# Performance work log

Hardware: AMD Instinct MI355X
Metric: run time of the kernel (lower is better)

Reference implementation:

```python
import jax, jax.numpy as jnp
import numpy as np
from functools import partial

EPS = 1e-5
TOP_K = 1
NUM_EXPERTS = 3
LOSS_COEF = 0.01


def conv2d(x, w, stride, pad):
    return jax.lax.conv_general_dilated(
        x, w, (stride, stride), [(pad, pad), (pad, pad)],
        dimension_numbers=("NCHW", "OIHW", "NCHW"))


def setup_inputs() -> dict:
    key = jax.random.key(0)
    ks = jax.random.split(key, 8)
    b, c, t, h, w = 8, 3, 5, 512, 512
    E = NUM_EXPERTS
    s = 0.05  # small init scale
    return {
        "x": jax.random.normal(ks[0], (b, c, t, h, w), jnp.float32),
        "g_conv_w": jax.random.normal(ks[1], (64, 15, 7, 7), jnp.float32) * s,
        "g_bn_gamma": jnp.ones((64,), jnp.float32),
        "g_bn_beta": jnp.zeros((64,), jnp.float32),
        "g_bn_mean": jnp.zeros((64,), jnp.float32),
        "g_bn_var": jnp.ones((64,), jnp.float32),
        "g_fc_w": jax.random.normal(ks[2], (E, 64), jnp.float32) * s,
        "g_fc_b": jnp.zeros((E,), jnp.float32),
        "e_conv1_w": jax.random.normal(ks[3], (E, 64, 15, 7, 7), jnp.float32) * s,
        "e_conv2_w": jax.random.normal(ks[4], (E, 128, 64, 3, 3), jnp.float32) * s,
        "e_head_w1": jax.random.normal(ks[5], (E, 128, 128, 3, 3), jnp.float32) * s,
        "e_head_b1": jnp.zeros((E, 128), jnp.float32),
        "e_head_w2": jax.random.normal(ks[6], (E, 5, 128, 1, 1), jnp.float32) * s,
        "e_head_b2": jnp.zeros((E, 5), jnp.float32),
    }


def gating(xr, g_conv_w, g_bn_gamma, g_bn_beta, g_bn_mean, g_bn_var, g_fc_w, g_fc_b):
    # backbone: conv 7x7 s2 -> BN (eval) -> ReLU -> maxpool 3x3 s2 -> GAP -> fc
    f = conv2d(xr, g_conv_w, 2, 3)
    scale = g_bn_gamma / jnp.sqrt(g_bn_var + EPS)
    f = f * scale[None, :, None, None] + (g_bn_beta - g_bn_mean * scale)[None, :, None, None]
    f = jax.nn.relu(f)
    f = jax.lax.reduce_window(f, -jnp.inf, jax.lax.max, (1, 1, 3, 3), (1, 1, 2, 2),
                              [(0, 0), (0, 0), (1, 1), (1, 1)])
    pooled = f.mean(axis=(2, 3))                       # (b, 64)
    logits = pooled @ g_fc_w.T + g_fc_b                # (b, E)
    b = logits.shape[0]
    _, top_idx = jax.lax.top_k(logits, TOP_K)          # (b, k)
    rows = jnp.arange(b)[:, None]
    # eval-mode gating: uniform 1/k over selected experts
    sparse_gates = jnp.zeros_like(logits).at[rows, top_idx].set(1.0 / TOP_K)
    expert_mask = jnp.zeros_like(logits).at[rows, top_idx].set(1.0)
    density = expert_mask.mean(axis=0)
    density_proxy = jax.nn.softmax(logits, axis=1).mean(axis=0)
    aux_loss = (density * density_proxy).sum() * NUM_EXPERTS
    return sparse_gates, aux_loss


def expert_forward(xr, w1, w2, hw1, hb1, hw2, hb2):
    y = jax.nn.relu(conv2d(xr, w1, 2, 3))              # (b, 64, H/2, W/2)
    y = jax.nn.relu(conv2d(y, w2, 2, 1))               # (b, 128, H/4, W/4)
    y = jax.nn.relu(conv2d(y, hw1, 1, 1) + hb1[None, :, None, None])
    y = conv2d(y, hw2, 1, 0) + hb2[None, :, None, None]  # (b, 5, H/4, W/4)
    return y


def reference(x, g_conv_w, g_bn_gamma, g_bn_beta, g_bn_mean, g_bn_var, g_fc_w, g_fc_b,
              e_conv1_w, e_conv2_w, e_head_w1, e_head_b1, e_head_w2, e_head_b2):
    b, c, t, h, w = x.shape
    xr = x.reshape(b, c * t, h, w)
    sparse_gates, aux_loss = gating(xr, g_conv_w, g_bn_gamma, g_bn_beta,
                                    g_bn_mean, g_bn_var, g_fc_w, g_fc_b)
    # run all experts (gates are 0 for unselected -> identical math to sparse dispatch)
    outs = jax.vmap(lambda w1, w2, hw1, hb1, hw2, hb2:
                    expert_forward(xr, w1, w2, hw1, hb1, hw2, hb2))(
        e_conv1_w, e_conv2_w, e_head_w1, e_head_b1, e_head_w2, e_head_b2)  # (E,b,5,h4,w4)
    combined = jnp.einsum("ebchw,be->bchw", outs, sparse_gates)
    hm, wh, reg = combined[:, 0:1], combined[:, 1:3], combined[:, 3:5]
    return hm, wh, reg, LOSS_COEF * aux_loss
```

## Files before the change

kernel.cpp:

```cpp
#include <hip/hip_runtime.h>
#include <cstdint>
#include <cmath>


typedef _Float16 f16x8 __attribute__((ext_vector_type(8)));
typedef _Float16 f16x4 __attribute__((ext_vector_type(4)));
typedef float f32x4 __attribute__((ext_vector_type(4)));

__device__ __forceinline__ void g2l16(const void* g, void* l) {
  __builtin_amdgcn_global_load_lds((__attribute__((address_space(1))) void*)g,
                                   (__attribute__((address_space(3))) void*)l,
                                   16, 0, 0);
}

__device__ __forceinline__ int xcd_swz(int bid, int nwg) {
  return (bid & 7) * (nwg >> 3) + (bid >> 3);
}

__global__ __launch_bounds__(256) void prep_x_k(
    const float* __restrict__ x, _Float16* __restrict__ xp)
{
  const int t = blockIdx.x * 256 + threadIdx.x;
  const int pix = t & 262143;
  const int b   = t >> 18;
  const float* src = x + (size_t)b * 15 * 262144 + pix;
  f16x8 lo, hi;
#pragma unroll
  for (int c = 0; c < 8; ++c)  lo[c] = (_Float16)src[(size_t)c * 262144];
#pragma unroll
  for (int c = 8; c < 15; ++c) hi[c - 8] = (_Float16)src[(size_t)c * 262144];
  hi[7] = (_Float16)0.f;
  *(f16x8*)&xp[(size_t)t * 16]     = lo;
  *(f16x8*)&xp[(size_t)t * 16 + 8] = hi;
}

__global__ __launch_bounds__(256) void prep_w7_k(
    const float* __restrict__ gw, const float* __restrict__ ew,
    _Float16* __restrict__ wp)
{
  const int i = blockIdx.x * 256 + threadIdx.x;
  const int kk   = i & 31;
  const int cout = (i >> 5) & 63;
  const int pair = (i >> 11) & 3;
  const int v    = i >> 13;
  const int ky = v % 7, set = v / 7;
  const int t = kk >> 4, cin = kk & 15;
  const int kx = 2 * pair + t;
  float val = 0.f;
  if (cin < 15 && kx < 7) {
    if (set == 0) val = gw[((cout * 15 + cin) * 7 + ky) * 7 + kx];
    else          val = ew[((((set - 1) * 64 + cout) * 15 + cin) * 7 + ky) * 7 + kx];
  }
  wp[i] = (_Float16)val;
}

template<int CINC>
__global__ __launch_bounds__(256) void prep_w3_k(
    const float* __restrict__ w, _Float16* __restrict__ wp)
{
  constexpr int CH = CINC / 32;
  const int i = blockIdx.x * 256 + threadIdx.x;
  const int kk   = i & 31;
  const int cout = (i >> 5) & 127;
  int rest = i >> 12;
  const int ch  = rest % CH;  rest /= CH;
  const int tap = rest % 9;
  const int e   = rest / 9;
  const int cin = ch * 32 + kk;
  wp[i] = (_Float16)w[((size_t)(e * 128 + cout) * CINC + cin) * 9 + tap];
}

template<int MODE>
__global__ __launch_bounds__(256, 3) void conv7m_k(
    const _Float16* __restrict__ xp, const _Float16* __restrict__ wp,
    const float* __restrict__ bn_g, const float* __restrict__ bn_b,
    const float* __restrict__ bn_m, const float* __restrict__ bn_v,
    const int* __restrict__ sel, _Float16* __restrict__ out)
{
  constexpr int ROWF = 518 * 16;
  __shared__ __align__(16) _Float16 smem[18432];
  const int sb = xcd_swz(blockIdx.x, 2048);
  const int oy = sb & 255, b = sb >> 8;
  const int wv = threadIdx.x >> 6, lane = threadIdx.x & 63;
  const int ln15 = lane & 15, quad = lane >> 4;
  const int npx0 = wv * 64;

  int set = 0;
  if constexpr (MODE == 1) set = 1 + sel[b];
  const _Float16* wset = wp + (size_t)set * (7 * 4 * 64 * 32);
  const _Float16* xb   = xp + (size_t)b * (512 * 512 * 16);

  const _Float16* xrow[7];
  bool rowok[7];
#pragma unroll
  for (int ky = 0; ky < 7; ++ky) {
    const int iy = 2 * oy - 3 + ky;
    rowok[ky] = (unsigned)iy < 512u;
    const int iyc = iy < 0 ? 0 : (iy > 511 ? 511 : iy);
    xrow[ky] = xb + (size_t)iyc * (512 * 16);
  }

  if (threadIdx.x < 32) {
    const int bi = threadIdx.x >> 4, k = threadIdx.x & 15;
    if (k < 12) {
      const int g = (k < 6) ? k : (1030 + k - 6);
      f16x8 z = {};
      *(f16x8*)&smem[bi * ROWF + g * 8] = z;
    }
  }

  f32x4 acc[4][4];
#pragma unroll
  for (int f = 0; f < 4; ++f)
#pragma unroll
    for (int g = 0; g < 4; ++g) acc[f][g] = (f32x4){0.f, 0.f, 0.f, 0.f};

  auto load_af = [&](int t, f16x8* af) {
    const int ky = t >> 2, pair = t & 3;
    const _Float16* wt = wset + (size_t)((ky * 4 + pair) * 64) * 32;
#pragma unroll
    for (int f = 0; f < 4; ++f)
      af[f] = *(const f16x8*)&wt[(f * 16 + ln15) * 32 + quad * 8];
  };
  auto stage = [&](int ky, int bi) {
    _Float16* bufb = &smem[bi * ROWF];
    const _Float16* xr = xrow[ky];
#pragma unroll
    for (int s = 0; s < 4; ++s) {
      const int seg = wv * 4 + s;
      const int gl = 6 + seg * 64 + lane;
      const int gs = gl ^ ((gl >> 3) & 7);
      g2l16(xr + (size_t)((gs >> 1) - 3) * 16 + (gs & 1) * 8,
            bufb + (6 + seg * 64) * 8);
    }
  };

  int gb[4];
#pragma unroll
  for (int g = 0; g < 4; ++g)
    gb[g] = 4 * (npx0 + g * 16 + ln15) + quad;

  f16x8 afb[3][4];
  load_af(0, afb[0]);
  load_af(1, afb[1]);
  stage(0, 0);
  __syncthreads();

#pragma unroll
  for (int t = 0; t < 28; ++t) {
    const int ky = t >> 2, pair = t & 3;
    const int cur = ky & 1;
    if (t + 2 < 28) load_af(t + 2, afb[(t + 2) % 3]);
    if (pair == 0 && ky + 1 < 7) stage(ky + 1, cur ^ 1);
    if (rowok[ky]) {
      const _Float16* bufb = &smem[cur * ROWF];
#pragma unroll
      for (int g = 0; g < 4; ++g) {
        const int gq = gb[g] + 4 * pair;
        const int gs = gq ^ ((gq >> 3) & 7);
        const f16x8 bf = *(const f16x8*)&bufb[gs * 8];
#pragma unroll
        for (int f = 0; f < 4; ++f)
          acc[f][g] = __builtin_amdgcn_mfma_f32_16x16x32_f16(afb[t % 3][f], bf, acc[f][g], 0, 0, 0);
      }
    }
    if (pair == 3) __syncthreads();
  }

  _Float16* sw = &smem[wv * 4608];
#pragma unroll
  for (int f = 0; f < 4; ++f) {
    float scl[4], add[4];
#pragma unroll
    for (int r = 0; r < 4; ++r) {
      const int cout = f * 16 + quad * 4 + r;
      if constexpr (MODE == 0) {
        const float sc = bn_g[cout] * rsqrtf(bn_v[cout] + 1e-5f);
        scl[r] = sc; add[r] = bn_b[cout] - bn_m[cout] * sc;
      } else { scl[r] = 1.f; add[r] = 0.f; }
    }
#pragma unroll
    for (int g = 0; g < 4; ++g) {
      f16x4 h;
#pragma unroll
      for (int r = 0; r < 4; ++r)
        h[r] = (_Float16)fmaxf(acc[f][g][r] * scl[r] + add[r], 0.f);
      *(f16x4*)&sw[(g * 16 + ln15) * 72 + f * 16 + quad * 4] = h;
    }
  }
  __syncthreads();
  const size_t rowbase = ((size_t)(b * 256 + oy) * 256 + npx0) * 64;
#pragma unroll
  for (int i = 0; i < 8; ++i) {
    const int pxl = (lane >> 3) + i * 8;
    const int c8  = (lane & 7) * 8;
    const f16x8 v = *(const f16x8*)&sw[pxl * 72 + c8];
    *(f16x8*)&out[rowbase + (size_t)pxl * 64 + c8] = v;
  }
}

template<int CINC, int S, int INSZ, int OUTSZ, int MODE>
__global__ __launch_bounds__(256, 3) void conv3m_k(
    const _Float16* __restrict__ xp, const _Float16* __restrict__ wp,
    const float* __restrict__ p_bias, const int* __restrict__ sel,
    _Float16* __restrict__ out)
{
  constexpr int CH  = CINC / 32;
  constexpr int NCH = 3 * CH;
  constexpr int NT  = NCH * 3;
  constexpr int NPX = (S == 1) ? (OUTSZ + 2) : (2 * OUTSZ + 1);
  constexpr int ROWF = NPX * 32;
  constexpr int NGR  = NPX * 4;
  constexpr int SPW  = INSZ / 64;
  __shared__ __align__(16) _Float16 smem[18432];
  const int sb = xcd_swz(blockIdx.x, OUTSZ * 8);
  const int oy = sb % OUTSZ, b = sb / OUTSZ;
  const int wv = threadIdx.x >> 6, lane = threadIdx.x & 63;
  const int ln15 = lane & 15, quad = lane >> 4;
  const int mwb = (wv >> 1) * 64, nwb = (wv & 1) * 64;

  const int e = sel[b];
  const _Float16* we = wp + (size_t)e * (9 * CH * 128 * 32);
  const _Float16* xb = xp + (size_t)b * ((size_t)INSZ * INSZ * CINC);

  const _Float16* xrow[3];
  bool rowok[3];
#pragma unroll
  for (int ky = 0; ky < 3; ++ky) {
    const int iy = S * oy + ky - 1;
    rowok[ky] = (unsigned)iy < (unsigned)INSZ;
    const int iyc = iy < 0 ? 0 : (iy >= INSZ ? INSZ - 1 : iy);
    xrow[ky] = xb + (size_t)iyc * INSZ * CINC;
  }

  {
    constexpr int HGPB = (S == 1) ? 8 : 4;
    if (threadIdx.x < 2 * HGPB) {
      const int bi = threadIdx.x / HGPB, k = threadIdx.x % HGPB;
      const int g = (k < 4) ? k : (NGR - 8 + k);
      f16x8 z = {};
      *(f16x8*)&smem[bi * ROWF + g * 8] = z;
    }
  }

  f32x4 acc[4][4];
#pragma unroll
  for (int f = 0; f < 4; ++f)
#pragma unroll
    for (int g = 0; g < 4; ++g) acc[f][g] = (f32x4){0.f, 0.f, 0.f, 0.f};

  auto load_af = [&](int t, f16x8* af) {
    const int c = t / 3, kx = t % 3;
    const int ky = c / CH, ch = c % CH;
    const _Float16* wt = we + (size_t)(((ky * 3 + kx) * CH + ch) * 128) * 32;
#pragma unroll
    for (int f = 0; f < 4; ++f)
      af[f] = *(const f16x8*)&wt[(mwb + f * 16 + ln15) * 32 + quad * 8];
  };
  auto stage = [&](int c, int bi) {
    const int ky = c / CH, ch = c % CH;
    _Float16* bufb = &smem[bi * ROWF];
    const _Float16* xr = xrow[ky];
#pragma unroll
    for (int s = 0; s < SPW; ++s) {
      const int seg = wv * SPW + s;
      const int gl = 4 + seg * 64 + lane;
      const int gs = gl ^ ((gl >> 3) & 7);
      g2l16(xr + (size_t)((gs >> 2) - 1) * CINC + ch * 32 + (gs & 3) * 8,
            bufb + (4 + seg * 64) * 8);
    }
  };

  int gb[4];
#pragma unroll
  for (int g = 0; g < 4; ++g) {
    const int ox = nwb + g * 16 + ln15;
    gb[g] = 4 * S * ox + quad;
  }

  f16x8 afb[3][4];
  load_af(0, afb[0]);
  load_af(1, afb[1]);
  stage(0, 0);
  __syncthreads();

#pragma unroll
  for (int t = 0; t < NT; ++t) {
    const int c = t / 3, kx = t % 3;
    const int ky = c / CH;
    const int cur = c & 1;
    if (t + 2 < NT) load_af(t + 2, afb[(t + 2) % 3]);
    if (kx == 0 && c + 1 < NCH) stage(c + 1, cur ^ 1);
    if (rowok[ky]) {
      const _Float16* bufb = &smem[cur * ROWF];
#pragma unroll
      for (int g = 0; g < 4; ++g) {
        const int gq = gb[g] + 4 * kx;
        const int gs = gq ^ ((gq >> 3) & 7);
        const f16x8 bf = *(const f16x8*)&bufb[gs * 8];
#pragma unroll
        for (int f = 0; f < 4; ++f)
          acc[f][g] = __builtin_amdgcn_mfma_f32_16x16x32_f16(afb[t % 3][f], bf, acc[f][g], 0, 0, 0);
      }
    }
    if (kx == 2) __syncthreads();
  }

  _Float16* sw = &smem[wv * 4608];
#pragma unroll
  for (int f = 0; f < 4; ++f) {
#pragma unroll
    for (int g = 0; g < 4; ++g) {
      f16x4 h;
#pragma unroll
      for (int r = 0; r < 4; ++r) {
        const int cout = mwb + f * 16 + quad * 4 + r;
        float v = acc[f][g][r];
        if constexpr (MODE == 2) v += p_bias[e * 128 + cout];
        h[r] = (_Float16)fmaxf(v, 0.f);
      }
      *(f16x4*)&sw[(g * 16 + ln15) * 72 + f * 16 + quad * 4] = h;
    }
  }
  __syncthreads();
  const size_t rowbase = ((size_t)(b * OUTSZ + oy) * OUTSZ + nwb) * 128 + mwb;
#pragma unroll
  for (int i = 0; i < 8; ++i) {
    const int pxl = (lane >> 3) + i * 8;
    const int c8  = (lane & 7) * 8;
    const f16x8 v = *(const f16x8*)&sw[pxl * 72 + c8];
    *(f16x8*)&out[rowbase + (size_t)pxl * 128 + c8] = v;
  }
}

__global__ void zero_k(float* __restrict__ pooled) {
  if (threadIdx.x < 512) pooled[threadIdx.x] = 0.f;
}

__global__ __launch_bounds__(256) void pool_k(
    const _Float16* __restrict__ f, float* __restrict__ pooled)
{
  const int sb = xcd_swz(blockIdx.x, 1024);
  const int b  = sb >> 7;
  const int py = sb & 127;
  const int wv = threadIdx.x >> 6, lane = threadIdx.x & 63;
  const int c8  = (lane & 7) * 8;
  const int pxq = lane >> 3;
  const _Float16* fb = f + (size_t)b * 256 * 256 * 64;

  const int y0 = 2 * py - 1;
  float s[8];
#pragma unroll
  for (int j = 0; j < 8; ++j) s[j] = 0.f;

#pragma unroll
  for (int step = 0; step < 4; ++step) {
    const int px = wv * 32 + step * 8 + pxq;
    const int x0 = 2 * px - 1;
    f16x8 m;
#pragma unroll
    for (int j = 0; j < 8; ++j) m[j] = (_Float16)(-60000.f);
#pragma unroll
    for (int dy = 0; dy < 3; ++dy) {
      const int y = y0 + dy;
      if ((unsigned)y < 256u) {
        const _Float16* row = fb + (size_t)y * 256 * 64 + c8;
        if (x0 >= 0)
          m = __builtin_elementwise_max(m, *(const f16x8*)&row[(size_t)x0 * 64]);
        m = __builtin_elementwise_max(m, *(const f16x8*)&row[(size_t)(x0 + 1) * 64]);
        m = __builtin_elementwise_max(m, *(const f16x8*)&row[(size_t)(x0 + 2) * 64]);
      }
    }
#pragma unroll
    for (int j = 0; j < 8; ++j) s[j] += (float)m[j];
  }

  __shared__ float red[256][8];
#pragma unroll
  for (int j = 0; j < 8; ++j) red[threadIdx.x][j] = s[j];
  __syncthreads();
  if (threadIdx.x < 64) {
    const int c = threadIdx.x, cg = c >> 3, cj = c & 7;
    float t = 0.f;
#pragma unroll
    for (int k = 0; k < 32; ++k)
      t += red[(k >> 3) * 64 + (k & 7) * 8 + cg][cj];
    atomicAdd(&pooled[b * 64 + c], t);
  }
}

__global__ __launch_bounds__(64) void gate_k(
    const float* __restrict__ pooled, const float* __restrict__ fcw,
    const float* __restrict__ fcb, int* __restrict__ sel, float* __restrict__ out_aux)
{
  __shared__ float probs[8][3];
  __shared__ int sidx[8];
  const int b = threadIdx.x;
  if (b < 8) {
    float l[3];
#pragma unroll
    for (int e = 0; e < 3; ++e) {
      float s = fcb[e];
      for (int c = 0; c < 64; ++c)
        s = fmaf(pooled[b * 64 + c] * (1.f / 16384.f), fcw[e * 64 + c], s);
      l[e] = s;
    }
    int best = 0;
    if (l[1] > l[best]) best = 1;
    if (l[2] > l[best]) best = 2;
    sel[b] = best;
    sidx[b] = best;
    const float m = fmaxf(l[0], fmaxf(l[1], l[2]));
    const float e0 = expf(l[0] - m), e1 = expf(l[1] - m), e2 = expf(l[2] - m);
    const float inv = 1.f / (e0 + e1 + e2);
    probs[b][0] = e0 * inv; probs[b][1] = e1 * inv; probs[b][2] = e2 * inv;
  }
  __syncthreads();
  if (threadIdx.x == 0) {
    float cnt[3] = {0.f, 0.f, 0.f}, pr[3] = {0.f, 0.f, 0.f};
    for (int bb = 0; bb < 8; ++bb) {
      cnt[sidx[bb]] += 1.f;
#pragma unroll
      for (int e = 0; e < 3; ++e) pr[e] += probs[bb][e];
    }
    float aux = 0.f;
#pragma unroll
    for (int e = 0; e < 3; ++e) aux += (cnt[e] * 0.125f) * (pr[e] * 0.125f);
    *out_aux = 0.01f * (3.f * aux);
  }
}

__global__ __launch_bounds__(256) void head2m_k(
    const _Float16* __restrict__ in, const float* __restrict__ w,
    const float* __restrict__ b2, const int* __restrict__ sel,
    float* __restrict__ out)
{
  const int b = blockIdx.x >> 6;
  const int p = ((blockIdx.x & 63) << 8) + threadIdx.x;
  const int e = sel[b];
  const float* wp = w + (size_t)e * 5 * 128;
  const _Float16* ip = in + ((size_t)(b << 14) + p) * 128;
  float a0 = 0.f, a1 = 0.f, a2 = 0.f, a3 = 0.f, a4 = 0.f;
#pragma unroll
  for (int cc = 0; cc < 16; ++cc) {
    const f16x8 v8 = *(const f16x8*)&ip[cc * 8];
#pragma unroll
    for (int j = 0; j < 8; ++j) {
      const float v = (float)v8[j];
      const int c = cc * 8 + j;
      a0 = fmaf(v, wp[c], a0);
      a1 = fmaf(v, wp[128 + c], a1);
      a2 = fmaf(v, wp[256 + c], a2);
      a3 = fmaf(v, wp[384 + c], a3);
      a4 = fmaf(v, wp[512 + c], a4);
    }
  }
  a0 += b2[e * 5 + 0]; a1 += b2[e * 5 + 1]; a2 += b2[e * 5 + 2];
  a3 += b2[e * 5 + 3]; a4 += b2[e * 5 + 4];
  out[(b << 14) + p] = a0;
  out[131072 + ((b * 2 + 0) << 14) + p] = a1;
  out[131072 + ((b * 2 + 1) << 14) + p] = a2;
  out[393216 + ((b * 2 + 0) << 14) + p] = a3;
  out[393216 + ((b * 2 + 1) << 14) + p] = a4;
}

extern "C" void kernel_launch(void* const* d_in, const int* in_sizes, int n_in,
                              void* d_out, int out_size, void* d_ws, size_t ws_size,
                              hipStream_t stream) {
  const float* x          = (const float*)d_in[0];
  const float* g_conv_w   = (const float*)d_in[1];
  const float* g_bn_gamma = (const float*)d_in[2];
  const float* g_bn_beta  = (const float*)d_in[3];
  const float* g_bn_mean  = (const float*)d_in[4];
  const float* g_bn_var   = (const float*)d_in[5];
  const float* g_fc_w     = (const float*)d_in[6];
  const float* g_fc_b     = (const float*)d_in[7];
  const float* e_conv1_w  = (const float*)d_in[8];
  const float* e_conv2_w  = (const float*)d_in[9];
  const float* e_head_w1  = (const float*)d_in[10];
  const float* e_head_b1  = (const float*)d_in[11];
  const float* e_head_w2  = (const float*)d_in[12];
  const float* e_head_b2  = (const float*)d_in[13];
  float* out = (float*)d_out;

  _Float16* xp      = (_Float16*)d_ws;
  _Float16* featbuf = xp + 33554432;
  _Float16* y2      = featbuf + 33554432;
  _Float16* w7p     = y2 + 16777216;
  _Float16* w2p     = w7p + 229376;
  _Float16* w3p     = w2p + 221184;
  _Float16* y3      = xp;
  float*    pooled  = (float*)(w3p + 442368);
  int*      sel     = (int*)(pooled + 512);

  prep_x_k<<<8192, 256, 0, stream>>>(x, xp);
  prep_w7_k<<<896, 256, 0, stream>>>(g_conv_w, e_conv1_w, w7p);
  prep_w3_k<64><<<864, 256, 0, stream>>>(e_conv2_w, w2p);
  prep_w3_k<128><<<1728, 256, 0, stream>>>(e_head_w1, w3p);
  zero_k<<<1, 512, 0, stream>>>(pooled);

  conv7m_k<0><<<2048, 256, 0, stream>>>(xp, w7p, g_bn_gamma, g_bn_beta,
                                        g_bn_mean, g_bn_var, nullptr, featbuf);
  pool_k<<<1024, 256, 0, stream>>>(featbuf, pooled);
  gate_k<<<1, 64, 0, stream>>>(pooled, g_fc_w, g_fc_b, sel, out + 655360);

  conv7m_k<1><<<2048, 256, 0, stream>>>(xp, w7p, nullptr, nullptr, nullptr, nullptr,
                                        sel, featbuf);
  conv3m_k<64, 2, 256, 128, 1><<<1024, 256, 0, stream>>>(featbuf, w2p, nullptr, sel, y2);
  conv3m_k<128, 1, 128, 128, 2><<<1024, 256, 0, stream>>>(y2, w3p, e_head_b1, sel, y3);
  head2m_k<<<512, 256, 0, stream>>>(y3, e_head_w2, e_head_b2, sel, out);
}
```

Baseline: 495.9 us.

## Quad-buffer LDS input rows in conv kernels and halve barrier count

Both conv kernels now use four LDS row buffers instead of two, staging two input rows ahead and synchronising once every two rows instead of every row. The 7x7 kernel also drops its XCD block swizzle and moves from triple- to double-buffered weight fragments, prefetching one step ahead. The goal is fewer barriers and more latency hiding for the global-to-LDS loads. In exchange LDS use per block grows (4*518*16 halves, about 66KB for conv7), which may cut occupancy below the three blocks per CU requested. Removing the swizzle may also hurt L2 locality.

```diff
diff --git a/kernel.cpp b/kernel.cpp
--- a/kernel.cpp
+++ b/kernel.cpp
@@ -78,9 +78,8 @@
     const int* __restrict__ sel, _Float16* __restrict__ out)
 {
   constexpr int ROWF = 518 * 16;
-  __shared__ __align__(16) _Float16 smem[18432];
-  const int sb = xcd_swz(blockIdx.x, 2048);
-  const int oy = sb & 255, b = sb >> 8;
+  __shared__ __align__(16) _Float16 smem[4 * ROWF];
+  const int oy = blockIdx.x & 255, b = blockIdx.x >> 8;
   const int wv = threadIdx.x >> 6, lane = threadIdx.x & 63;
   const int ln15 = lane & 15, quad = lane >> 4;
   const int npx0 = wv * 64;
@@ -100,7 +99,7 @@
     xrow[ky] = xb + (size_t)iyc * (512 * 16);
   }
 
-  if (threadIdx.x < 32) {
+  if (threadIdx.x < 64) {
     const int bi = threadIdx.x >> 4, k = threadIdx.x & 15;
     if (k < 12) {
       const int g = (k < 6) ? k : (1030 + k - 6);
@@ -140,18 +139,23 @@
   for (int g = 0; g < 4; ++g)
     gb[g] = 4 * (npx0 + g * 16 + ln15) + quad;
 
-  f16x8 afb[3][4];
-  load_af(0, afb[0]);
-  load_af(1, afb[1]);
+  f16x8 afA[4], afB[4];
+  load_af(0, afA);
   stage(0, 0);
+  stage(1, 1);
   __syncthreads();
 
 #pragma unroll
   for (int t = 0; t < 28; ++t) {
     const int ky = t >> 2, pair = t & 3;
-    const int cur = ky & 1;
-    if (t + 2 < 28) load_af(t + 2, afb[(t + 2) % 3]);
-    if (pair == 0 && ky + 1 < 7) stage(ky + 1, cur ^ 1);
+    const int cur = ky & 3;
+    f16x8* afc = (t & 1) ? afB : afA;
+    f16x8* afn = (t & 1) ? afA : afB;
+    if (t + 1 < 28) load_af(t + 1, afn);
+    if (pair == 0 && (ky & 1) == 0) {
+      if (ky + 2 < 7) stage(ky + 2, (ky + 2) & 3);
+      if (ky + 3 < 7) stage(ky + 3, (ky + 3) & 3);
+    }
     if (rowok[ky]) {
       const _Float16* bufb = &smem[cur * ROWF];
 #pragma unroll
@@ -161,11 +165,12 @@
         const f16x8 bf = *(const f16x8*)&bufb[gs * 8];
 #pragma unroll
         for (int f = 0; f < 4; ++f)
-          acc[f][g] = __builtin_amdgcn_mfma_f32_16x16x32_f16(afb[t % 3][f], bf, acc[f][g], 0, 0, 0);
+          acc[f][g] = __builtin_amdgcn_mfma_f32_16x16x32_f16(afc[f], bf, acc[f][g], 0, 0, 0);
       }
     }
-    if (pair == 3) __syncthreads();
-  }
+    if (pair == 3 && (ky & 1)) __syncthreads();
+  }
+  __syncthreads();
 
   _Float16* sw = &smem[wv * 4608];
 #pragma unroll
@@ -212,7 +217,8 @@
   constexpr int ROWF = NPX * 32;
   constexpr int NGR  = NPX * 4;
   constexpr int SPW  = INSZ / 64;
-  __shared__ __align__(16) _Float16 smem[18432];
+  constexpr int SMEMF = (4 * ROWF > 18432) ? 4 * ROWF : 18432;
+  __shared__ __align__(16) _Float16 smem[SMEMF];
   const int sb = xcd_swz(blockIdx.x, OUTSZ * 8);
   const int oy = sb % OUTSZ, b = sb / OUTSZ;
   const int wv = threadIdx.x >> 6, lane = threadIdx.x & 63;
@@ -235,7 +241,7 @@
 
   {
     constexpr int HGPB = (S == 1) ? 8 : 4;
-    if (threadIdx.x < 2 * HGPB) {
+    if (threadIdx.x < 4 * HGPB) {
       const int bi = threadIdx.x / HGPB, k = threadIdx.x % HGPB;
       const int g = (k < 4) ? k : (NGR - 8 + k);
       f16x8 z = {};
@@ -282,15 +288,19 @@
   load_af(0, afb[0]);
   load_af(1, afb[1]);
   stage(0, 0);
+  stage(1, 1);
   __syncthreads();
 
 #pragma unroll
   for (int t = 0; t < NT; ++t) {
     const int c = t / 3, kx = t % 3;
     const int ky = c / CH;
-    const int cur = c & 1;
+    const int cur = c & 3;
     if (t + 2 < NT) load_af(t + 2, afb[(t + 2) % 3]);
-    if (kx == 0 && c + 1 < NCH) stage(c + 1, cur ^ 1);
+    if (kx == 0 && (c & 1) == 0) {
+      if (c + 2 < NCH) stage(c + 2, (c + 2) & 3);
+      if (c + 3 < NCH) stage(c + 3, (c + 3) & 3);
+    }
     if (rowok[ky]) {
       const _Float16* bufb = &smem[cur * ROWF];
 #pragma unroll
@@ -303,7 +313,7 @@
           acc[f][g] = __builtin_amdgcn_mfma_f32_16x16x32_f16(afb[t % 3][f], bf, acc[f][g], 0, 0, 0);
       }
     }
-    if (kx == 2) __syncthreads();
+    if (kx == 2 && (c & 1)) __syncthreads();
   }
 
   _Float16* sw = &smem[wv * 4608];
```

Measured after the change: 490.3 us. About the same (-1.1%).
